# Kernel tuning notes

Measured on AMD Instinct MI355X. Metric: run time of the kernel, lower is better.

Reference implementation:

```python
import jax, jax.numpy as jnp
import numpy as np


def setup_inputs() -> dict:
    key = jax.random.key(0)
    k1, k2, k3, k4 = jax.random.split(key, 4)
    bs, N, J, n_feat, n_out = 32, 512, 4, 64, 128
    X = jax.random.normal(k1, (bs, n_feat, N), dtype=jnp.float32)
    W = jax.random.normal(k2, (bs, N, N, J), dtype=jnp.float32)
    # Conv1d(J*n_feat, n_out, kernel_size=1) weights, init N(0, 0.1)
    fc_w = 0.1 * jax.random.normal(k3, (n_out, J * n_feat), dtype=jnp.float32)
    fc_b = 0.1 * jax.random.normal(k4, (n_out,), dtype=jnp.float32)
    mask = jnp.ones((bs, N), dtype=jnp.float32)  # unused by forward, kept for signature parity
    return {"X": X, "W": W, "fc_w": fc_w, "fc_b": fc_b, "N_batch": 32, "mask": mask}


def reference(X, W, fc_w, fc_b, N_batch, mask):
    bs, n_feat, N = X.shape
    J = W.shape[3]
    # graph_oper: out[b, j*n_feat+f, n] = sum_m W[b,n,m,j] * X[b,f,m]
    gx = jnp.einsum('bnmj,bfm->bjfn', W, X)            # [bs, J, n_feat, N]
    x1 = gx.reshape(bs, J * n_feat, N)                  # [bs, J*n_feat, N]
    # Conv1d with kernel size 1 == pointwise linear over channel dim
    y1 = jnp.einsum('oc,bcn->bon', fc_w, x1) + fc_b[None, :, None]  # [bs, n_out, N]
    y = jnp.sum(y1, axis=2)                             # [bs, n_out]
    return y
```

## Files before the change

kernel.cpp:

```cpp
#include <hip/hip_runtime.h>

#define BS   32
#define NF   64
#define NN   512
#define JJ   4
#define NOUT 128
#define CC   256
#define NC   16
#define ROWS 32
#define MJC  2
#define ROW4 512
#define CH4  256

__global__ __launch_bounds__(256) void sumW_kernel(const float4* __restrict__ W4,
                                                   float4* __restrict__ P4) {
    int blk  = blockIdx.x;
    int mjc  = blk & (MJC - 1);
    int rest = blk >> 1;
    int nc   = rest & (NC - 1);
    int b    = rest >> 4;
    int m    = mjc * CH4 + threadIdx.x;

    const float4* p = W4 + ((size_t)(b * NN + nc * ROWS)) * ROW4 + m;
    float4 acc = make_float4(0.f, 0.f, 0.f, 0.f);
#pragma unroll 8
    for (int r = 0; r < ROWS; ++r) {
        float4 v = p[(size_t)r * ROW4];
        acc.x += v.x; acc.y += v.y; acc.z += v.z; acc.w += v.w;
    }
    P4[((size_t)(b * NC + nc)) * ROW4 + m] = acc;
}

__global__ __launch_bounds__(256) void finish_kernel(const float4* __restrict__ P4,
                                                     const float4* __restrict__ X4,
                                                     const float4* __restrict__ fcw4,
                                                     const float* __restrict__ fcb,
                                                     float* __restrict__ out) {
    __shared__ __align__(16) float S[JJ][4][132];
    __shared__ __align__(16) float Tp[4][CC];
    __shared__ __align__(16) float4 Tsum4[CC / 4];

    int b = blockIdx.x;
    int t = threadIdx.x;

    for (int m = t; m < NN; m += 256) {
        float4 a = make_float4(0.f, 0.f, 0.f, 0.f);
#pragma unroll
        for (int nc = 0; nc < NC; ++nc) {
            float4 v = P4[((size_t)(b * NC + nc)) * ROW4 + m];
            a.x += v.x; a.y += v.y; a.z += v.z; a.w += v.w;
        }
        int ms = m >> 7, mr = m & 127;
        S[0][ms][mr] = a.x; S[1][ms][mr] = a.y; S[2][ms][mr] = a.z; S[3][ms][mr] = a.w;
    }
    __syncthreads();

    int f = t >> 2, ms = t & 3;
    const float4* xp = X4 + ((size_t)(b * NF + f)) * (NN / 4) + ms * 32;
    const float4* s0 = (const float4*)(&S[0][ms][0]);
    const float4* s1 = (const float4*)(&S[1][ms][0]);
    const float4* s2 = (const float4*)(&S[2][ms][0]);
    const float4* s3 = (const float4*)(&S[3][ms][0]);
    float t0 = 0.f, t1 = 0.f, t2 = 0.f, t3 = 0.f;
#pragma unroll 4
    for (int i = 0; i < 32; ++i) {
        float4 xv = xp[i];
        float4 a0 = s0[i], a1 = s1[i], a2 = s2[i], a3 = s3[i];
        t0 += xv.x * a0.x + xv.y * a0.y + xv.z * a0.z + xv.w * a0.w;
        t1 += xv.x * a1.x + xv.y * a1.y + xv.z * a1.z + xv.w * a1.w;
        t2 += xv.x * a2.x + xv.y * a2.y + xv.z * a2.z + xv.w * a2.w;
        t3 += xv.x * a3.x + xv.y * a3.y + xv.z * a3.z + xv.w * a3.w;
    }
    Tp[ms][0 * NF + f] = t0;
    Tp[ms][1 * NF + f] = t1;
    Tp[ms][2 * NF + f] = t2;
    Tp[ms][3 * NF + f] = t3;
    __syncthreads();

    if (t < CC / 4) {
        const float4* r0 = (const float4*)Tp[0];
        const float4* r1 = (const float4*)Tp[1];
        const float4* r2 = (const float4*)Tp[2];
        const float4* r3 = (const float4*)Tp[3];
        float4 a = r0[t], b1 = r1[t], c = r2[t], d = r3[t];
        Tsum4[t] = make_float4(a.x + b1.x + c.x + d.x,
                               a.y + b1.y + c.y + d.y,
                               a.z + b1.z + c.z + d.z,
                               a.w + b1.w + c.w + d.w);
    }
    __syncthreads();

    if (t < NOUT) {
        float acc = (float)NN * fcb[t];
#pragma unroll 8
        for (int i = 0; i < CC / 4; ++i) {
            float4 wv = fcw4[(size_t)t * (CC / 4) + i];
            float4 sv = Tsum4[i];
            acc += wv.x * sv.x + wv.y * sv.y + wv.z * sv.z + wv.w * sv.w;
        }
        out[b * NOUT + t] = acc;
    }
}

extern "C" void kernel_launch(void* const* d_in, const int* in_sizes, int n_in,
                              void* d_out, int out_size, void* d_ws, size_t ws_size,
                              hipStream_t stream) {
    const float4* X4   = (const float4*)d_in[0];
    const float4* W4   = (const float4*)d_in[1];
    const float4* fcw4 = (const float4*)d_in[2];
    const float*  fcb  = (const float*)d_in[3];
    float* out = (float*)d_out;

    float4* P4 = (float4*)d_ws;

    sumW_kernel<<<BS * NC * MJC, 256, 0, stream>>>(W4, P4);
    finish_kernel<<<BS, 256, 0, stream>>>(P4, X4, fcw4, fcb, out);
}
```

Before: 215.7 us.

## Fuse W row-sum with X/fc contraction per chunk and combine via atomics

Each block now sums its 32-row chunk of W, then directly contracts that partial sum with X and fc_w, and atomically adds the result into the output. A small kernel first writes the bias term into the output. This removes the workspace round trip and the serial 32-block finish stage, in exchange for redundant X/fc_w reads per chunk, 512 blocks instead of 1024 for the bandwidth-bound W pass, and float atomics whose summation order is nondeterministic.

```diff
diff --git a/kernel.cpp b/kernel.cpp
--- a/kernel.cpp
+++ b/kernel.cpp
@@ -8,50 +8,43 @@
 #define CC   256
 #define NC   16
 #define ROWS 32
-#define MJC  2
 #define ROW4 512
-#define CH4  256
 
-__global__ __launch_bounds__(256) void sumW_kernel(const float4* __restrict__ W4,
-                                                   float4* __restrict__ P4) {
-    int blk  = blockIdx.x;
-    int mjc  = blk & (MJC - 1);
-    int rest = blk >> 1;
-    int nc   = rest & (NC - 1);
-    int b    = rest >> 4;
-    int m    = mjc * CH4 + threadIdx.x;
-
-    const float4* p = W4 + ((size_t)(b * NN + nc * ROWS)) * ROW4 + m;
-    float4 acc = make_float4(0.f, 0.f, 0.f, 0.f);
-#pragma unroll 8
-    for (int r = 0; r < ROWS; ++r) {
-        float4 v = p[(size_t)r * ROW4];
-        acc.x += v.x; acc.y += v.y; acc.z += v.z; acc.w += v.w;
-    }
-    P4[((size_t)(b * NC + nc)) * ROW4 + m] = acc;
+__global__ __launch_bounds__(256) void bias_init_kernel(const float* __restrict__ fcb,
+                                                        float* __restrict__ out) {
+    int i = blockIdx.x * 256 + threadIdx.x;
+    out[i] = (float)NN * fcb[i & (NOUT - 1)];
 }
 
-__global__ __launch_bounds__(256) void finish_kernel(const float4* __restrict__ P4,
-                                                     const float4* __restrict__ X4,
-                                                     const float4* __restrict__ fcw4,
-                                                     const float* __restrict__ fcb,
-                                                     float* __restrict__ out) {
+__global__ __launch_bounds__(256) void fused_kernel(const float4* __restrict__ W4,
+                                                    const float4* __restrict__ X4,
+                                                    const float4* __restrict__ fcw4,
+                                                    float* __restrict__ out) {
     __shared__ __align__(16) float S[JJ][4][132];
     __shared__ __align__(16) float Tp[4][CC];
     __shared__ __align__(16) float4 Tsum4[CC / 4];
 
-    int b = blockIdx.x;
-    int t = threadIdx.x;
+    int blk = blockIdx.x;
+    int nc  = blk & (NC - 1);
+    int b   = blk >> 4;
+    int t   = threadIdx.x;
 
-    for (int m = t; m < NN; m += 256) {
-        float4 a = make_float4(0.f, 0.f, 0.f, 0.f);
-#pragma unroll
-        for (int nc = 0; nc < NC; ++nc) {
-            float4 v = P4[((size_t)(b * NC + nc)) * ROW4 + m];
-            a.x += v.x; a.y += v.y; a.z += v.z; a.w += v.w;
-        }
-        int ms = m >> 7, mr = m & 127;
-        S[0][ms][mr] = a.x; S[1][ms][mr] = a.y; S[2][ms][mr] = a.z; S[3][ms][mr] = a.w;
+    const float4* p = W4 + ((size_t)(b * NN + nc * ROWS)) * ROW4 + t;
+    float4 a0 = make_float4(0.f, 0.f, 0.f, 0.f);
+    float4 a1 = make_float4(0.f, 0.f, 0.f, 0.f);
+#pragma unroll 8
+    for (int r = 0; r < ROWS; ++r) {
+        float4 v0 = p[(size_t)r * ROW4];
+        float4 v1 = p[(size_t)r * ROW4 + 256];
+        a0.x += v0.x; a0.y += v0.y; a0.z += v0.z; a0.w += v0.w;
+        a1.x += v1.x; a1.y += v1.y; a1.z += v1.z; a1.w += v1.w;
+    }
+    {
+        int ms = t >> 7, mr = t & 127;
+        S[0][ms][mr] = a0.x; S[1][ms][mr] = a0.y;
+        S[2][ms][mr] = a0.z; S[3][ms][mr] = a0.w;
+        S[0][ms + 2][mr] = a1.x; S[1][ms + 2][mr] = a1.y;
+        S[2][ms + 2][mr] = a1.z; S[3][ms + 2][mr] = a1.w;
     }
     __syncthreads();
 
@@ -65,11 +58,11 @@
 #pragma unroll 4
     for (int i = 0; i < 32; ++i) {
         float4 xv = xp[i];
-        float4 a0 = s0[i], a1 = s1[i], a2 = s2[i], a3 = s3[i];
-        t0 += xv.x * a0.x + xv.y * a0.y + xv.z * a0.z + xv.w * a0.w;
-        t1 += xv.x * a1.x + xv.y * a1.y + xv.z * a1.z + xv.w * a1.w;
-        t2 += xv.x * a2.x + xv.y * a2.y + xv.z * a2.z + xv.w * a2.w;
-        t3 += xv.x * a3.x + xv.y * a3.y + xv.z * a3.z + xv.w * a3.w;
+        float4 b0 = s0[i], b1 = s1[i], b2 = s2[i], b3 = s3[i];
+        t0 += xv.x * b0.x + xv.y * b0.y + xv.z * b0.z + xv.w * b0.w;
+        t1 += xv.x * b1.x + xv.y * b1.y + xv.z * b1.z + xv.w * b1.w;
+        t2 += xv.x * b2.x + xv.y * b2.y + xv.z * b2.z + xv.w * b2.w;
+        t3 += xv.x * b3.x + xv.y * b3.y + xv.z * b3.z + xv.w * b3.w;
     }
     Tp[ms][0 * NF + f] = t0;
     Tp[ms][1 * NF + f] = t1;
@@ -82,23 +75,23 @@
         const float4* r1 = (const float4*)Tp[1];
         const float4* r2 = (const float4*)Tp[2];
         const float4* r3 = (const float4*)Tp[3];
-        float4 a = r0[t], b1 = r1[t], c = r2[t], d = r3[t];
-        Tsum4[t] = make_float4(a.x + b1.x + c.x + d.x,
-                               a.y + b1.y + c.y + d.y,
-                               a.z + b1.z + c.z + d.z,
-                               a.w + b1.w + c.w + d.w);
+        float4 x0 = r0[t], x1 = r1[t], x2 = r2[t], x3 = r3[t];
+        Tsum4[t] = make_float4(x0.x + x1.x + x2.x + x3.x,
+                               x0.y + x1.y + x2.y + x3.y,
+                               x0.z + x1.z + x2.z + x3.z,
+                               x0.w + x1.w + x2.w + x3.w);
     }
     __syncthreads();
 
     if (t < NOUT) {
-        float acc = (float)NN * fcb[t];
+        float acc = 0.f;
 #pragma unroll 8
         for (int i = 0; i < CC / 4; ++i) {
             float4 wv = fcw4[(size_t)t * (CC / 4) + i];
             float4 sv = Tsum4[i];
             acc += wv.x * sv.x + wv.y * sv.y + wv.z * sv.z + wv.w * sv.w;
         }
-        out[b * NOUT + t] = acc;
+        atomicAdd(&out[b * NOUT + t], acc);
     }
 }
 
@@ -111,8 +104,6 @@
     const float*  fcb  = (const float*)d_in[3];
     float* out = (float*)d_out;
 
-    float4* P4 = (float4*)d_ws;
-
-    sumW_kernel<<<BS * NC * MJC, 256, 0, stream>>>(W4, P4);
-    finish_kernel<<<BS, 256, 0, stream>>>(P4, X4, fcw4, fcb, out);
+    bias_init_kernel<<<(BS * NOUT) / 256, 256, 0, stream>>>(fcb, out);
+    fused_kernel<<<BS * NC, 256, 0, stream>>>(W4, X4, fcw4, out);
 }
```

After: 222.5 us. +3.1%, slower.
